# Kernel optimization log

Measured on AMD Instinct MI355X. Metric: run time of the kernel, lower is better.

## Reference

```python
import jax, jax.numpy as jnp
import numpy as np

HEADS = 8
CH = 256
DH = CH // HEADS  # 32
NB = 128          # nb_features
EPS = 1e-4


def setup_inputs() -> dict:
    key = jax.random.key(0)
    ks = jax.random.split(key, 8)
    b, c, h, w = 4, CH, 96, 96
    s = 1.0 / np.sqrt(CH)  # typical linear init scale
    x = jax.random.normal(ks[0], (b, c, h, w), dtype=jnp.float32)
    wq = jax.random.normal(ks[1], (CH, CH), dtype=jnp.float32) * s
    wk = jax.random.normal(ks[2], (CH, CH), dtype=jnp.float32) * s
    wv = jax.random.normal(ks[3], (CH, CH), dtype=jnp.float32) * s
    wo = jax.random.normal(ks[4], (CH, CH), dtype=jnp.float32) * s
    bo = jnp.zeros((CH,), dtype=jnp.float32)
    # FAVOR+ gaussian orthogonal random projection (nb_features, dim_head)
    pm = np.random.default_rng(0)
    blocks = []
    for _ in range(NB // DH):
        qmat, _ = np.linalg.qr(pm.standard_normal((DH, DH)))
        blocks.append(qmat.T)
    proj = np.concatenate(blocks, axis=0)
    # scale rows to chi-distributed norms (scaling=0 default in performer_pytorch)
    norms = np.linalg.norm(pm.standard_normal((NB, DH)), axis=1, keepdims=True)
    proj_mat = jnp.asarray(proj * norms, dtype=jnp.float32)
    wp = jax.random.normal(ks[5], (CH, CH, 1, 1), dtype=jnp.float32) * s
    bp = jnp.zeros((CH,), dtype=jnp.float32)
    return {"x": x, "wq": wq, "wk": wk, "wv": wv, "wo": wo, "bo": bo,
            "proj_mat": proj_mat, "wp": wp, "bp": bp}


def softmax_kernel(data, proj, is_query):
    # data: (b, h, n, d); proj: (m, d). Performer FAVOR+ positive softmax features.
    data_normalizer = data.shape[-1] ** -0.25
    ratio = proj.shape[0] ** -0.5
    data_dash = jnp.einsum('bhnd,md->bhnm', data * data_normalizer, proj)
    diag = (jnp.sum(data * data, axis=-1) * 0.5 * (data_normalizer ** 2))[..., None]
    if is_query:
        m = jnp.max(data_dash, axis=-1, keepdims=True)
    else:
        m = jnp.max(data_dash, axis=(-1, -2), keepdims=True)
    return ratio * (jnp.exp(data_dash - diag - m) + EPS)


def reference(x, wq, wk, wv, wo, bo, proj_mat, wp, bp):
    b, c, h, w = x.shape
    n = h * w
    xf = x.reshape(b, c, n).transpose(0, 2, 1)  # (b, n, c)

    def split_heads(t):
        return t.reshape(b, n, HEADS, DH).transpose(0, 2, 1, 3)  # (b, h, n, d)

    q = split_heads(xf @ wq.T)
    k = split_heads(xf @ wk.T)
    v = split_heads(xf @ wv.T)

    qp = softmax_kernel(q, proj_mat, True)   # (b, h, n, m)
    kp = softmax_kernel(k, proj_mat, False)  # (b, h, n, m)

    # non-causal linear attention
    k_sum = jnp.sum(kp, axis=-2)                                   # (b, h, m)
    d_inv = 1.0 / jnp.einsum('bhnm,bhm->bhn', qp, k_sum)           # (b, h, n)
    ctx = jnp.einsum('bhnm,bhnd->bhmd', kp, v)                     # (b, h, m, d)
    out = jnp.einsum('bhnm,bhmd->bhnd', qp, ctx) * d_inv[..., None]

    out = out.transpose(0, 2, 1, 3).reshape(b, n, c)  # merge heads
    out = out @ wo.T + bo                              # to_out (attn_out_bias=True)
    out = out.transpose(0, 2, 1).reshape(b, c, h, w)
    # 1x1 conv projection
    out = jnp.einsum('bchw,oc->bohw', out, wp[:, :, 0, 0]) + bp[None, :, None, None]
    return out
```

## Files before the change

kernel.cpp:

```cpp
#include <hip/hip_runtime.h>

#define NTOT 9216
#define NORMC 0.42044820762685725f
#define RATIO 0.08838834764831845f
#define FEPS 1e-4f

typedef _Float16 h8 __attribute__((ext_vector_type(8)));
typedef _Float16 h4 __attribute__((ext_vector_type(4)));
typedef float f4 __attribute__((ext_vector_type(4)));

__device__ __forceinline__ void gld16(const _Float16* g, _Float16* l) {
  __builtin_amdgcn_global_load_lds((const __attribute__((address_space(1))) void*)g,
                                   (__attribute__((address_space(3))) void*)l, 16, 0, 0);
}

__global__ __launch_bounds__(256) void prep(
    const float* __restrict__ x, const float* __restrict__ wq,
    const float* __restrict__ wk, const float* __restrict__ wv,
    const float* __restrict__ proj, const float* __restrict__ wo,
    const float* __restrict__ bo, const float* __restrict__ wp,
    const float* __restrict__ bp, _Float16* __restrict__ xT,
    _Float16* __restrict__ Wall, _Float16* __restrict__ projh,
    _Float16* __restrict__ Wc, float* __restrict__ bc) {
  __shared__ float T_s[64][65];
  int r = blockIdx.x, t = threadIdx.x;
  if (r < 2304) {
    int nx = r % 144, rem = r / 144;
    int cy = rem & 3, b = rem >> 2;
    int n0 = nx * 64, c0 = cy * 64;
    for (int i = 0; i < 4; ++i) {
      int f = t + i * 256;
      int cc = f >> 4, n4 = f & 15;
      float4 a = *(const float4*)(x + ((size_t)(b * 256 + c0 + cc)) * NTOT + n0 + n4 * 4);
      T_s[cc][n4 * 4 + 0] = a.x;
      T_s[cc][n4 * 4 + 1] = a.y;
      T_s[cc][n4 * 4 + 2] = a.z;
      T_s[cc][n4 * 4 + 3] = a.w;
    }
    __syncthreads();
    for (int i = 0; i < 2; ++i) {
      int f = t + i * 256;
      int nn = f >> 3, c8 = f & 7;
      h8 hv;
      for (int j = 0; j < 8; ++j) hv[j] = (_Float16)T_s[c8 * 8 + j][nn];
      *(h8*)(xT + ((size_t)(b * NTOT + n0 + nn)) * 256 + c0 + c8 * 8) = hv;
    }
    return;
  }
  int r2 = r - 2304;
  if (r2 < 768) {
    const float* src = (r2 < 256) ? wq + (size_t)r2 * 256
                     : (r2 < 512) ? wk + (size_t)(r2 - 256) * 256
                                  : wv + (size_t)(r2 - 512) * 256;
    Wall[(size_t)r2 * 256 + t] = (_Float16)src[t];
  } else if (r2 < 784) {
    int idx = (r2 - 768) * 256 + t;
    projh[idx] = (_Float16)proj[idx];
  } else {
    int o = r2 - 784;
    float acc = 0.f;
    for (int c = 0; c < 256; ++c) acc += wp[o * 256 + c] * wo[c * 256 + t];
    Wc[o * 256 + t] = (_Float16)acc;
    if (t == 0) {
      float ab = bp[o];
      for (int c = 0; c < 256; ++c) ab += wp[o * 256 + c] * bo[c];
      bc[o] = ab;
    }
  }
}

__global__ __launch_bounds__(256) void qkv_mfma(
    const _Float16* __restrict__ xT, const _Float16* __restrict__ Wall,
    const _Float16* __restrict__ projh, _Float16* __restrict__ q,
    _Float16* __restrict__ k, _Float16* __restrict__ vT,
    float* __restrict__ kmaxp) {
  __shared__ __align__(16) _Float16 pool[16384];
  int bx = blockIdx.x, co0 = blockIdx.y * 128, sel = blockIdx.z;
  int b = bx / 72, ntile = bx % 72;
  int n0 = bx * 128;
  const _Float16* Wb = Wall + (size_t)sel * 65536;
  int t = threadIdx.x, wave = t >> 6, lane = t & 63;
  int lm = lane & 15, lg = lane >> 4;
  int wm = (wave & 1) * 64, wn = (wave >> 1) * 64;
  int srow = wave * 32 + (lane >> 2);
  int scol = ((lane & 3) ^ ((lane >> 3) & 3)) * 8;
  const _Float16* gA = Wb + (size_t)(co0 + srow) * 256 + scol;
  const _Float16* gB = xT + (size_t)(n0 + srow) * 256 + scol;
  int so = wave * 1024;
  int pg = (lg ^ ((lm >> 1) & 3)) * 8;
  f4 acc[4][4] = {};
  gld16(gA, pool + so);
  gld16(gA + 16 * 256, pool + so + 512);
  gld16(gB, pool + 8192 + so);
  gld16(gB + 16 * 256, pool + 8192 + so + 512);
  __syncthreads();
#pragma unroll
  for (int kt = 0; kt < 8; ++kt) {
    int cur = (kt & 1) << 12;
    int nxt = cur ^ 4096;
    if (kt < 7) {
      int c0 = (kt + 1) * 32;
      gld16(gA + c0, pool + nxt + so);
      gld16(gA + c0 + 16 * 256, pool + nxt + so + 512);
      gld16(gB + c0, pool + 8192 + nxt + so);
      gld16(gB + c0 + 16 * 256, pool + 8192 + nxt + so + 512);
    }
    h8 a[4], bf[4];
#pragma unroll
    for (int mi = 0; mi < 4; ++mi)
      a[mi] = *(const h8*)&pool[cur + (wm + mi * 16 + lm) * 32 + pg];
#pragma unroll
    for (int ni = 0; ni < 4; ++ni)
      bf[ni] = *(const h8*)&pool[8192 + cur + (wn + ni * 16 + lm) * 32 + pg];
    if (sel < 2) {
#pragma unroll
      for (int mi = 0; mi < 4; ++mi)
#pragma unroll
        for (int ni = 0; ni < 4; ++ni)
          acc[mi][ni] = __builtin_amdgcn_mfma_f32_16x16x32_f16(a[mi], bf[ni], acc[mi][ni], 0, 0, 0);
    } else {
#pragma unroll
      for (int mi = 0; mi < 4; ++mi)
#pragma unroll
        for (int ni = 0; ni < 4; ++ni)
          acc[mi][ni] = __builtin_amdgcn_mfma_f32_16x16x32_f16(bf[ni], a[mi], acc[mi][ni], 0, 0, 0);
    }
    __syncthreads();
  }
  if (sel < 2) {
    _Float16* Out = (sel == 0) ? q : k;
#pragma unroll
    for (int mi = 0; mi < 4; ++mi)
#pragma unroll
      for (int ni = 0; ni < 4; ++ni) {
        h4 hv;
#pragma unroll
        for (int r = 0; r < 4; ++r) hv[r] = (_Float16)acc[mi][ni][r];
        *(h4*)(Out + (size_t)(n0 + wn + ni * 16 + lm) * 256 + co0 + wm + mi * 16 + lg * 4) = hv;
      }
    if (sel == 1) {
      _Float16* ktile = pool;
      h8 pr[8];
#pragma unroll
      for (int mt = 0; mt < 8; ++mt)
        pr[mt] = *(const h8*)&projh[(mt * 16 + lm) * 32 + lg * 8];
      float vmax = -1e30f;
      for (int half = 0; half < 2; ++half) {
        __syncthreads();
        if ((wave >> 1) == half) {
#pragma unroll
          for (int mi = 0; mi < 4; ++mi)
#pragma unroll
            for (int ni = 0; ni < 4; ++ni) {
              h4 hv;
#pragma unroll
              for (int r = 0; r < 4; ++r) hv[r] = (_Float16)acc[mi][ni][r];
              *(h4*)&ktile[(ni * 16 + lm) * 132 + wm + mi * 16 + lg * 4] = hv;
            }
        }
        __syncthreads();
#pragma unroll
        for (int nt2 = 0; nt2 < 4; ++nt2) {
          h8 a = *(const h8*)&ktile[(nt2 * 16 + lm) * 132 + wave * 32 + lg * 8];
#pragma unroll
          for (int mt = 0; mt < 8; ++mt) {
            f4 z = {0.f, 0.f, 0.f, 0.f};
            f4 d = __builtin_amdgcn_mfma_f32_16x16x32_f16(a, pr[mt], z, 0, 0, 0);
            vmax = fmaxf(vmax, fmaxf(fmaxf(d[0], d[1]), fmaxf(d[2], d[3])));
          }
        }
      }
      for (int i = 1; i < 64; i <<= 1) vmax = fmaxf(vmax, __shfl_xor(vmax, i, 64));
      if (lane == 0) {
        int h = (co0 >> 5) + wave;
        kmaxp[(size_t)(b * 8 + h) * 72 + ntile] = NORMC * vmax;
      }
    }
  } else {
#pragma unroll
    for (int mi = 0; mi < 4; ++mi)
#pragma unroll
      for (int ni = 0; ni < 4; ++ni) {
        h4 hv;
#pragma unroll
        for (int r = 0; r < 4; ++r) hv[r] = (_Float16)acc[mi][ni][r];
        *(h4*)(vT + ((size_t)(b * 256 + co0 + wm + mi * 16 + lm)) * NTOT +
               ntile * 128 + wn + ni * 16 + lg * 4) = hv;
      }
  }
}

__global__ __launch_bounds__(256) void ctx_mfma(
    const _Float16* __restrict__ k, const _Float16* __restrict__ vT,
    const _Float16* __restrict__ projh, const float* __restrict__ kmaxp,
    float* __restrict__ part) {
  __shared__ __align__(16) _Float16 k_s[128 * 32];
  __shared__ __align__(16) _Float16 vT_s[32 * 136];
  __shared__ __align__(16) _Float16 kpT[128 * 136];
  __shared__ float diag_s[128];
  __shared__ float kmax_sh;
  int bh = blockIdx.y, b = bh >> 3, h = bh & 7;
  int nbase = blockIdx.x * 384;
  int t = threadIdx.x, wave = t >> 6, lane = t & 63, lm = lane & 15, lg = lane >> 4;
  h8 pr[8];
#pragma unroll
  for (int mt = 0; mt < 8; ++mt) pr[mt] = *(const h8*)&projh[(mt * 16 + lm) * 32 + lg * 8];
  int scol = ((lane & 3) ^ ((lane >> 3) & 3)) * 8;
  const _Float16* gK =
      k + ((size_t)(b * NTOT + nbase + wave * 32 + (lane >> 2))) * 256 + h * 32 + scol;
  const _Float16* gV = vT + ((size_t)(b * 256 + h * 32 + (t >> 3))) * NTOT + nbase;
  _Float16* lK = k_s + wave * 1024;
  gld16(gK, lK);
  gld16(gK + 16 * 256, lK + 512);
  {
    float* kred = (float*)kpT;
    if (t < 72) kred[t] = kmaxp[(size_t)bh * 72 + t];
    __syncthreads();
    if (t == 0) {
      float mx = -1e30f;
      for (int i = 0; i < 72; ++i) mx = fmaxf(mx, kred[i]);
      kmax_sh = mx;
    }
    __syncthreads();
  }
  float kmax = kmax_sh;
  int pg = (lg ^ ((lm >> 1) & 3)) * 8;
  f4 cacc[2][2] = {};
  float ks[8] = {};
  for (int ch = 0; ch < 3; ++ch) {
    {
      int d = t >> 3, g = t & 7;
#pragma unroll
      for (int i = 0; i < 2; ++i)
        *(h8*)&vT_s[d * 136 + (i * 8 + g) * 8] = *(const h8*)(gV + ch * 128 + (i * 8 + g) * 8);
    }
    __syncthreads();
    if (t < 128) {
      float s = 0.f;
#pragma unroll
      for (int c = 0; c < 4; ++c) {
        h8 kv = *(const h8*)&k_s[t * 32 + c * 8];
#pragma unroll
        for (int j = 0; j < 8; ++j) s += (float)kv[j] * (float)kv[j];
      }
      diag_s[t] = s * (0.5f * NORMC * NORMC);
    }
    f4 dsh[2][8];
#pragma unroll
    for (int nt = 0; nt < 2; ++nt) {
      h8 a = *(const h8*)&k_s[(wave * 32 + nt * 16 + lm) * 32 + pg];
#pragma unroll
      for (int mt = 0; mt < 8; ++mt) {
        f4 z = {0.f, 0.f, 0.f, 0.f};
        dsh[nt][mt] = __builtin_amdgcn_mfma_f32_16x16x32_f16(a, pr[mt], z, 0, 0, 0);
      }
    }
    __syncthreads();
    if (ch < 2) {
      gld16(gK + (size_t)((ch + 1) * 128) * 256, lK);
      gld16(gK + (size_t)((ch + 1) * 128) * 256 + 16 * 256, lK + 512);
    }
#pragma unroll
    for (int nt = 0; nt < 2; ++nt)
#pragma unroll
      for (int mt = 0; mt < 8; ++mt) {
        h4 hv;
        float lsum = 0.f;
#pragma unroll
        for (int r = 0; r < 4; ++r) {
          int nl = wave * 32 + nt * 16 + lg * 4 + r;
          float val = RATIO * (__expf(NORMC * dsh[nt][mt][r] - diag_s[nl] - kmax) + FEPS);
          hv[r] = (_Float16)val;
          lsum += val;
        }
        ks[mt] += lsum;
        *(h4*)&kpT[(mt * 16 + lm) * 136 + wave * 32 + nt * 16 + lg * 4] = hv;
      }
    __syncthreads();
#pragma unroll
    for (int k2 = 0; k2 < 4; ++k2) {
      h8 a2[2], b2[2];
#pragma unroll
      for (int mt2 = 0; mt2 < 2; ++mt2)
        a2[mt2] = *(const h8*)&kpT[(wave * 32 + mt2 * 16 + lm) * 136 + k2 * 32 + lg * 8];
#pragma unroll
      for (int dt = 0; dt < 2; ++dt)
        b2[dt] = *(const h8*)&vT_s[(dt * 16 + lm) * 136 + k2 * 32 + lg * 8];
#pragma unroll
      for (int mt2 = 0; mt2 < 2; ++mt2)
#pragma unroll
        for (int dt = 0; dt < 2; ++dt)
          cacc[mt2][dt] =
              __builtin_amdgcn_mfma_f32_16x16x32_f16(a2[mt2], b2[dt], cacc[mt2][dt], 0, 0, 0);
    }
    __syncthreads();
  }
  float* pp = part + (size_t)(blockIdx.y * 24 + blockIdx.x) * 4224;
#pragma unroll
  for (int mt2 = 0; mt2 < 2; ++mt2)
#pragma unroll
    for (int dt = 0; dt < 2; ++dt)
      *(f4*)(pp + (dt * 16 + lm) * 128 + wave * 32 + mt2 * 16 + lg * 4) = cacc[mt2][dt];
  float* redk = (float*)kpT;
#pragma unroll
  for (int mt = 0; mt < 8; ++mt) {
    float s = ks[mt];
    s += __shfl_xor(s, 16, 64);
    s += __shfl_xor(s, 32, 64);
    if (lg == 0) redk[wave * 128 + mt * 16 + lm] = s;
  }
  __syncthreads();
  if (t < 128)
    pp[32 * 128 + t] = redk[t] + redk[128 + t] + redk[256 + t] + redk[384 + t];
}

__global__ __launch_bounds__(256) void reduce_ctx(
    const float* __restrict__ part, _Float16* __restrict__ ctxT_g,
    float* __restrict__ ksum_g) {
  int bh = blockIdx.x >> 2, qtr = blockIdx.x & 3;
  int t = threadIdx.x;
  const float* pb = part + (size_t)bh * 24 * 4224;
  for (int it = 0; it < 5; ++it) {
    int lc = it * 256 + t;
    if (lc < 1056) {
      int cell = qtr * 1056 + lc;
      float s = 0.f;
      for (int p = 0; p < 24; ++p) s += pb[(size_t)p * 4224 + cell];
      int d = cell >> 7, m = cell & 127;
      if (d < 32) ctxT_g[(size_t)bh * 4096 + d * 128 + m] = (_Float16)s;
      else ksum_g[(size_t)bh * 128 + m] = s;
    }
  }
}

__global__ __launch_bounds__(256) void attn_mfma(
    const _Float16* __restrict__ q, const _Float16* __restrict__ projh,
    const _Float16* __restrict__ ctxT_g, const float* __restrict__ ksum_g,
    _Float16* __restrict__ attn) {
  __shared__ __align__(16) _Float16 q_sh[128 * 32];
  __shared__ __align__(16) _Float16 qp_s[128 * 136];
  __shared__ float ksum_s[128];
  int n0 = blockIdx.x * 128;
  int bh = blockIdx.y, b = bh >> 3, h = bh & 7;
  int t = threadIdx.x, wave = t >> 6, lane = t & 63, lm = lane & 15, lg = lane >> 4;
  h8 pr[8];
#pragma unroll
  for (int mt = 0; mt < 8; ++mt) pr[mt] = *(const h8*)&projh[(mt * 16 + lm) * 32 + lg * 8];
  int scol = ((lane & 3) ^ ((lane >> 3) & 3)) * 8;
  const _Float16* gQ =
      q + ((size_t)(b * NTOT + n0 + wave * 32 + (lane >> 2))) * 256 + h * 32 + scol;
  gld16(gQ, q_sh + wave * 1024);
  gld16(gQ + 16 * 256, q_sh + wave * 1024 + 512);
  h8 ac[2][4];
#pragma unroll
  for (int dt = 0; dt < 2; ++dt)
#pragma unroll
    for (int k2 = 0; k2 < 4; ++k2)
      ac[dt][k2] = *(const h8*)&ctxT_g[(size_t)bh * 4096 + (dt * 16 + lm) * 128 + k2 * 32 + lg * 8];
  if (t < 128) ksum_s[t] = ksum_g[(size_t)bh * 128 + t];
  __syncthreads();
  int pg = (lg ^ ((lm >> 1) & 3)) * 8;
  float diag_r[2];
#pragma unroll
  for (int nt = 0; nt < 2; ++nt) {
    int n = wave * 32 + nt * 16 + lm;
    float s = 0.f;
#pragma unroll
    for (int c = 0; c < 4; ++c) {
      h8 qv = *(const h8*)&q_sh[n * 32 + c * 8];
#pragma unroll
      for (int j = 0; j < 8; ++j) s += (float)qv[j] * (float)qv[j];
    }
    diag_r[nt] = s * (0.5f * NORMC * NORMC);
  }
  f4 dsh[2][8];
#pragma unroll
  for (int nt = 0; nt < 2; ++nt) {
    h8 qf = *(const h8*)&q_sh[(wave * 32 + nt * 16 + lm) * 32 + pg];
#pragma unroll
    for (int mt = 0; mt < 8; ++mt) {
      f4 z = {0.f, 0.f, 0.f, 0.f};
      dsh[nt][mt] = __builtin_amdgcn_mfma_f32_16x16x32_f16(pr[mt], qf, z, 0, 0, 0);
    }
  }
  float den_r[2];
#pragma unroll
  for (int nt = 0; nt < 2; ++nt) {
    float mx = -1e30f;
#pragma unroll
    for (int mt = 0; mt < 8; ++mt)
#pragma unroll
      for (int r = 0; r < 4; ++r) mx = fmaxf(mx, dsh[nt][mt][r]);
    mx = fmaxf(mx, __shfl_xor(mx, 16, 64));
    mx = fmaxf(mx, __shfl_xor(mx, 32, 64));
    float den = 0.f;
#pragma unroll
    for (int mt = 0; mt < 8; ++mt) {
      h4 hv;
#pragma unroll
      for (int r = 0; r < 4; ++r) {
        float val = RATIO * (__expf(NORMC * (dsh[nt][mt][r] - mx) - diag_r[nt]) + FEPS);
        hv[r] = (_Float16)val;
        den += val * ksum_s[mt * 16 + lg * 4 + r];
      }
      *(h4*)&qp_s[(wave * 32 + nt * 16 + lm) * 136 + mt * 16 + lg * 4] = hv;
    }
    den += __shfl_xor(den, 16, 64);
    den += __shfl_xor(den, 32, 64);
    den_r[nt] = 1.f / den;
  }
  __syncthreads();
  f4 oacc[2][2] = {};
#pragma unroll
  for (int k2 = 0; k2 < 4; ++k2) {
    h8 bq[2];
#pragma unroll
    for (int nt = 0; nt < 2; ++nt)
      bq[nt] = *(const h8*)&qp_s[(wave * 32 + nt * 16 + lm) * 136 + k2 * 32 + lg * 8];
#pragma unroll
    for (int dt = 0; dt < 2; ++dt)
#pragma unroll
      for (int nt = 0; nt < 2; ++nt)
        oacc[dt][nt] = __builtin_amdgcn_mfma_f32_16x16x32_f16(ac[dt][k2], bq[nt], oacc[dt][nt], 0, 0, 0);
  }
#pragma unroll
  for (int dt = 0; dt < 2; ++dt)
#pragma unroll
    for (int nt = 0; nt < 2; ++nt) {
      int n = wave * 32 + nt * 16 + lm;
      h4 hv;
#pragma unroll
      for (int r = 0; r < 4; ++r) hv[r] = (_Float16)(oacc[dt][nt][r] * den_r[nt]);
      *(h4*)(attn + ((size_t)(b * NTOT + n0 + n)) * 256 + h * 32 + dt * 16 + lg * 4) = hv;
    }
}

__global__ __launch_bounds__(256) void out_mfma(
    const _Float16* __restrict__ Wc, const _Float16* __restrict__ attn,
    const float* __restrict__ bc, float* __restrict__ out) {
  __shared__ __align__(16) _Float16 pool[16384];
  int bx = blockIdx.x;
  int o0 = blockIdx.y * 128;
  int b = bx / 72, nb0 = (bx % 72) * 128;
  int t = threadIdx.x, wave = t >> 6, lane = t & 63;
  int lm = lane & 15, lg = lane >> 4;
  int wm = (wave & 1) * 64, wn = (wave >> 1) * 64;
  int srow = wave * 32 + (lane >> 2);
  int scol = ((lane & 3) ^ ((lane >> 3) & 3)) * 8;
  const _Float16* gA = Wc + (size_t)(o0 + srow) * 256 + scol;
  const _Float16* gB = attn + (size_t)(b * NTOT + nb0 + srow) * 256 + scol;
  int so = wave * 1024;
  int pg = (lg ^ ((lm >> 1) & 3)) * 8;
  f4 acc[4][4] = {};
  gld16(gA, pool + so);
  gld16(gA + 16 * 256, pool + so + 512);
  gld16(gB, pool + 8192 + so);
  gld16(gB + 16 * 256, pool + 8192 + so + 512);
  __syncthreads();
#pragma unroll
  for (int kt = 0; kt < 8; ++kt) {
    int cur = (kt & 1) << 12;
    int nxt = cur ^ 4096;
    if (kt < 7) {
      int c0 = (kt + 1) * 32;
      gld16(gA + c0, pool + nxt + so);
      gld16(gA + c0 + 16 * 256, pool + nxt + so + 512);
      gld16(gB + c0, pool + 8192 + nxt + so);
      gld16(gB + c0 + 16 * 256, pool + 8192 + nxt + so + 512);
    }
    h8 a[4], bf[4];
#pragma unroll
    for (int mi = 0; mi < 4; ++mi)
      a[mi] = *(const h8*)&pool[cur + (wm + mi * 16 + lm) * 32 + pg];
#pragma unroll
    for (int ni = 0; ni < 4; ++ni)
      bf[ni] = *(const h8*)&pool[8192 + cur + (wn + ni * 16 + lm) * 32 + pg];
#pragma unroll
    for (int mi = 0; mi < 4; ++mi)
#pragma unroll
      for (int ni = 0; ni < 4; ++ni)
        acc[mi][ni] = __builtin_amdgcn_mfma_f32_16x16x32_f16(bf[ni], a[mi], acc[mi][ni], 0, 0, 0);
    __syncthreads();
  }
#pragma unroll
  for (int mi = 0; mi < 4; ++mi) {
    int o = o0 + wm + mi * 16 + lm;
    float bias = bc[o];
#pragma unroll
    for (int ni = 0; ni < 4; ++ni) {
      f4 ov = acc[mi][ni];
      float4 st = make_float4(ov[0] + bias, ov[1] + bias, ov[2] + bias, ov[3] + bias);
      *(float4*)(out + ((size_t)(b * 256 + o)) * NTOT + nb0 + wn + ni * 16 + lg * 4) = st;
    }
  }
}

extern "C" void kernel_launch(void* const* d_in, const int* in_sizes, int n_in,
                              void* d_out, int out_size, void* d_ws, size_t ws_size,
                              hipStream_t stream) {
  const float* x = (const float*)d_in[0];
  const float* wq = (const float*)d_in[1];
  const float* wk = (const float*)d_in[2];
  const float* wv = (const float*)d_in[3];
  const float* wo = (const float*)d_in[4];
  const float* bo = (const float*)d_in[5];
  const float* proj = (const float*)d_in[6];
  const float* wp = (const float*)d_in[7];
  const float* bp = (const float*)d_in[8];
  float* out = (float*)d_out;
  float* ws = (float*)d_ws;

  float* part = ws;
  float* kmaxp = part + 3244032;
  float* ksum_g = kmaxp + 2304;
  float* bc = ksum_g + 4096;
  _Float16* hb = (_Float16*)(bc + 256);
  const size_t THALF = (size_t)4 * NTOT * 256;
  _Float16* q_h = hb;
  _Float16* k_h = q_h + THALF;
  _Float16* xT = k_h + THALF;
  _Float16* vTg = xT + THALF;
  _Float16* Wall = vTg + THALF;
  _Float16* Wc = Wall + 768 * 256;
  _Float16* projh = Wc + 65536;
  _Float16* ctxT_g = projh + 4096;

  prep<<<3344, 256, 0, stream>>>(x, wq, wk, wv, proj, wo, bo, wp, bp,
                                 xT, Wall, projh, Wc, bc);
  qkv_mfma<<<dim3(288, 2, 3), 256, 0, stream>>>(xT, Wall, projh, q_h, k_h, vTg, kmaxp);
  ctx_mfma<<<dim3(24, 32), 256, 0, stream>>>(k_h, vTg, projh, kmaxp, part);
  reduce_ctx<<<128, 256, 0, stream>>>(part, ctxT_g, ksum_g);
  attn_mfma<<<dim3(72, 32), 256, 0, stream>>>(q_h, projh, ctxT_g, ksum_g, xT);
  out_mfma<<<dim3(288, 2), 256, 0, stream>>>(Wc, xT, bc, out);
}
```

Before: 219.7 us.

## Replace full syncthreads with partial vmcnt waits and prefetch V into registers

The QKV and output GEMM k-loops now issue the next tile's async LDS loads before waiting with s_waitcnt vmcnt(4). The current tile can then be consumed while the next one is still in flight, instead of draining all loads at each __syncthreads. The last iteration is peeled, and the loops are kept rolled. The context kernel prefetches the next V chunk into registers during compute and uses raw s_barrier with explicit waitcnts. This relies on hand-placed waitcnt counts being correct, which risks races if the compiler reorders or adds memory ops.

```diff
diff --git a/kernel.cpp b/kernel.cpp
--- a/kernel.cpp
+++ b/kernel.cpp
@@ -93,18 +93,18 @@
   gld16(gA + 16 * 256, pool + so + 512);
   gld16(gB, pool + 8192 + so);
   gld16(gB + 16 * 256, pool + 8192 + so + 512);
-  __syncthreads();
-#pragma unroll
-  for (int kt = 0; kt < 8; ++kt) {
+#pragma unroll 1
+  for (int kt = 0; kt < 7; ++kt) {
     int cur = (kt & 1) << 12;
     int nxt = cur ^ 4096;
-    if (kt < 7) {
-      int c0 = (kt + 1) * 32;
-      gld16(gA + c0, pool + nxt + so);
-      gld16(gA + c0 + 16 * 256, pool + nxt + so + 512);
-      gld16(gB + c0, pool + 8192 + nxt + so);
-      gld16(gB + c0 + 16 * 256, pool + 8192 + nxt + so + 512);
-    }
+    int c0 = (kt + 1) * 32;
+    gld16(gA + c0, pool + nxt + so);
+    gld16(gA + c0 + 16 * 256, pool + nxt + so + 512);
+    gld16(gB + c0, pool + 8192 + nxt + so);
+    gld16(gB + c0 + 16 * 256, pool + 8192 + nxt + so + 512);
+    asm volatile("s_waitcnt vmcnt(4)" ::: "memory");
+    __builtin_amdgcn_s_barrier();
+    __builtin_amdgcn_sched_barrier(0);
     h8 a[4], bf[4];
 #pragma unroll
     for (int mi = 0; mi < 4; ++mi)
@@ -125,7 +125,32 @@
         for (int ni = 0; ni < 4; ++ni)
           acc[mi][ni] = __builtin_amdgcn_mfma_f32_16x16x32_f16(bf[ni], a[mi], acc[mi][ni], 0, 0, 0);
     }
-    __syncthreads();
+    __builtin_amdgcn_s_barrier();
+  }
+  {
+    asm volatile("s_waitcnt vmcnt(0)" ::: "memory");
+    __builtin_amdgcn_s_barrier();
+    __builtin_amdgcn_sched_barrier(0);
+    h8 a[4], bf[4];
+#pragma unroll
+    for (int mi = 0; mi < 4; ++mi)
+      a[mi] = *(const h8*)&pool[4096 + (wm + mi * 16 + lm) * 32 + pg];
+#pragma unroll
+    for (int ni = 0; ni < 4; ++ni)
+      bf[ni] = *(const h8*)&pool[8192 + 4096 + (wn + ni * 16 + lm) * 32 + pg];
+    if (sel < 2) {
+#pragma unroll
+      for (int mi = 0; mi < 4; ++mi)
+#pragma unroll
+        for (int ni = 0; ni < 4; ++ni)
+          acc[mi][ni] = __builtin_amdgcn_mfma_f32_16x16x32_f16(a[mi], bf[ni], acc[mi][ni], 0, 0, 0);
+    } else {
+#pragma unroll
+      for (int mi = 0; mi < 4; ++mi)
+#pragma unroll
+        for (int ni = 0; ni < 4; ++ni)
+          acc[mi][ni] = __builtin_amdgcn_mfma_f32_16x16x32_f16(bf[ni], a[mi], acc[mi][ni], 0, 0, 0);
+    }
   }
   if (sel < 2) {
     _Float16* Out = (sel == 0) ? q : k;
@@ -210,8 +235,11 @@
       k + ((size_t)(b * NTOT + nbase + wave * 32 + (lane >> 2))) * 256 + h * 32 + scol;
   const _Float16* gV = vT + ((size_t)(b * 256 + h * 32 + (t >> 3))) * NTOT + nbase;
   _Float16* lK = k_s + wave * 1024;
+  int vd = t >> 3, vg = t & 7;
   gld16(gK, lK);
   gld16(gK + 16 * 256, lK + 512);
+  h8 vr0 = *(const h8*)(gV + vg * 8);
+  h8 vr1 = *(const h8*)(gV + 64 + vg * 8);
   {
     float* kred = (float*)kpT;
     if (t < 72) kred[t] = kmaxp[(size_t)bh * 72 + t];
@@ -227,14 +255,13 @@
   int pg = (lg ^ ((lm >> 1) & 3)) * 8;
   f4 cacc[2][2] = {};
   float ks[8] = {};
+#pragma unroll 1
   for (int ch = 0; ch < 3; ++ch) {
-    {
-      int d = t >> 3, g = t & 7;
-#pragma unroll
-      for (int i = 0; i < 2; ++i)
-        *(h8*)&vT_s[d * 136 + (i * 8 + g) * 8] = *(const h8*)(gV + ch * 128 + (i * 8 + g) * 8);
-    }
-    __syncthreads();
+    *(h8*)&vT_s[vd * 136 + vg * 8] = vr0;
+    *(h8*)&vT_s[vd * 136 + 64 + vg * 8] = vr1;
+    asm volatile("s_waitcnt vmcnt(0) lgkmcnt(0)" ::: "memory");
+    __builtin_amdgcn_s_barrier();
+    __builtin_amdgcn_sched_barrier(0);
     if (t < 128) {
       float s = 0.f;
 #pragma unroll
@@ -255,10 +282,14 @@
         dsh[nt][mt] = __builtin_amdgcn_mfma_f32_16x16x32_f16(a, pr[mt], z, 0, 0, 0);
       }
     }
-    __syncthreads();
+    asm volatile("s_waitcnt lgkmcnt(0)" ::: "memory");
+    __builtin_amdgcn_s_barrier();
+    __builtin_amdgcn_sched_barrier(0);
     if (ch < 2) {
       gld16(gK + (size_t)((ch + 1) * 128) * 256, lK);
       gld16(gK + (size_t)((ch + 1) * 128) * 256 + 16 * 256, lK + 512);
+      vr0 = *(const h8*)(gV + (ch + 1) * 128 + vg * 8);
+      vr1 = *(const h8*)(gV + (ch + 1) * 128 + 64 + vg * 8);
     }
 #pragma unroll
     for (int nt = 0; nt < 2; ++nt)
@@ -276,7 +307,9 @@
         ks[mt] += lsum;
         *(h4*)&kpT[(mt * 16 + lm) * 136 + wave * 32 + nt * 16 + lg * 4] = hv;
       }
-    __syncthreads();
+    asm volatile("s_waitcnt lgkmcnt(0)" ::: "memory");
+    __builtin_amdgcn_s_barrier();
+    __builtin_amdgcn_sched_barrier(0);
 #pragma unroll
     for (int k2 = 0; k2 < 4; ++k2) {
       h8 a2[2], b2[2];
@@ -293,7 +326,7 @@
           cacc[mt2][dt] =
               __builtin_amdgcn_mfma_f32_16x16x32_f16(a2[mt2], b2[dt], cacc[mt2][dt], 0, 0, 0);
     }
-    __syncthreads();
+    __builtin_amdgcn_s_barrier();
   }
   float* pp = part + (size_t)(blockIdx.y * 24 + blockIdx.x) * 4224;
 #pragma unroll
@@ -456,18 +489,18 @@
   gld16(gA + 16 * 256, pool + so + 512);
   gld16(gB, pool + 8192 + so);
   gld16(gB + 16 * 256, pool + 8192 + so + 512);
-  __syncthreads();
-#pragma unroll
-  for (int kt = 0; kt < 8; ++kt) {
+#pragma unroll 1
+  for (int kt = 0; kt < 7; ++kt) {
     int cur = (kt & 1) << 12;
     int nxt = cur ^ 4096;
-    if (kt < 7) {
-      int c0 = (kt + 1) * 32;
-      gld16(gA + c0, pool + nxt + so);
-      gld16(gA + c0 + 16 * 256, pool + nxt + so + 512);
-      gld16(gB + c0, pool + 8192 + nxt + so);
-      gld16(gB + c0 + 16 * 256, pool + 8192 + nxt + so + 512);
-    }
+    int c0 = (kt + 1) * 32;
+    gld16(gA + c0, pool + nxt + so);
+    gld16(gA + c0 + 16 * 256, pool + nxt + so + 512);
+    gld16(gB + c0, pool + 8192 + nxt + so);
+    gld16(gB + c0 + 16 * 256, pool + 8192 + nxt + so + 512);
+    asm volatile("s_waitcnt vmcnt(4)" ::: "memory");
+    __builtin_amdgcn_s_barrier();
+    __builtin_amdgcn_sched_barrier(0);
     h8 a[4], bf[4];
 #pragma unroll
     for (int mi = 0; mi < 4; ++mi)
@@ -480,7 +513,24 @@
 #pragma unroll
       for (int ni = 0; ni < 4; ++ni)
         acc[mi][ni] = __builtin_amdgcn_mfma_f32_16x16x32_f16(bf[ni], a[mi], acc[mi][ni], 0, 0, 0);
-    __syncthreads();
+    __builtin_amdgcn_s_barrier();
+  }
+  {
+    asm volatile("s_waitcnt vmcnt(0)" ::: "memory");
+    __builtin_amdgcn_s_barrier();
+    __builtin_amdgcn_sched_barrier(0);
+    h8 a[4], bf[4];
+#pragma unroll
+    for (int mi = 0; mi < 4; ++mi)
+      a[mi] = *(const h8*)&pool[4096 + (wm + mi * 16 + lm) * 32 + pg];
+#pragma unroll
+    for (int ni = 0; ni < 4; ++ni)
+      bf[ni] = *(const h8*)&pool[8192 + 4096 + (wn + ni * 16 + lm) * 32 + pg];
+#pragma unroll
+    for (int mi = 0; mi < 4; ++mi)
+#pragma unroll
+      for (int ni = 0; ni < 4; ++ni)
+        acc[mi][ni] = __builtin_amdgcn_mfma_f32_16x16x32_f16(bf[ni], a[mi], acc[mi][ni], 0, 0, 0);
   }
 #pragma unroll
   for (int mi = 0; mi < 4; ++mi) {
```

After: 217.1 us. Within noise of the previous version (-1.2%).
